# Kernel optimization log

Measured on AMD Instinct MI355X. Metric: run time of the kernel, lower is better.

The kernel has to match this reference:

```python
import jax, jax.numpy as jnp
import numpy as np
import math

# Config (matches init_kwargs): ProphetNet-style ngram self-attention
T, B, E, H, NGRAM, NB, MAXD = 512, 4, 1024, 16, 2, 32, 128
HD = E // H
TGT = (1 + NGRAM) * T
NEG = -1e9


def _buckets(rel):
    # faithful numpy version of _relative_positions_bucket (bidirectional=False)
    n = np.maximum(-rel, 0)
    max_exact = NB // 2
    is_small = n < max_exact
    large = max_exact + np.log(np.maximum(n, 1) / max_exact) / math.log(MAXD / max_exact) * (NB - max_exact)
    large = np.minimum(large, NB - 1).astype(np.int32)
    return np.where(is_small, n.astype(np.int32), large)


def setup_inputs() -> dict:
    key = jax.random.key(0)
    ks = jax.random.split(key, 4)
    s = 0.02
    # position ids 1..T (ProphetNet positions start at 1); precompute bucket tables
    pos = np.arange(1, T + 1, dtype=np.int64)[None, :].repeat(B, axis=0)          # [B,T]
    main_rel = pos[:, None, :] - pos[:, :, None]                                  # [B,T,T]
    pred_keys = np.concatenate([pos - 1, pos], axis=-1)                           # [B,2T]
    pred_rel = pred_keys[:, None, :] - pos[:, :, None]                            # [B,T,2T]
    return {
        "query": jax.random.normal(ks[0], (TGT, B, E), jnp.float32),
        "in_proj_weight": jax.random.normal(ks[1], (3 * E, E), jnp.float32) * s,
        "in_proj_bias": jnp.zeros((3 * E,), jnp.float32),
        "rel_w": jax.random.normal(ks[2], (NB * H, E), jnp.float32) * s,
        "rel_b": jnp.zeros((NB * H,), jnp.float32),
        "out_w": jax.random.normal(ks[3], (E, E), jnp.float32) * s,
        "out_b": jnp.zeros((E,), jnp.float32),
        "main_buckets": jnp.asarray(_buckets(main_rel), jnp.int32),
        "predict_buckets": jnp.asarray(_buckets(pred_rel), jnp.int32),
    }


def reference(query, in_proj_weight, in_proj_bias, rel_w, rel_b, out_w, out_b,
              main_buckets, predict_buckets):
    scaling = HD ** -0.5
    qkv = query @ in_proj_weight.T + in_proj_bias                  # [TGT,B,3E]
    q, k, v = jnp.split(qkv, 3, axis=-1)
    q = q * scaling

    def heads(x):  # [TGT,B,E] -> [B*H, TGT, HD]
        return x.reshape(TGT, B * H, HD).transpose(1, 0, 2)

    q, k, v = heads(q), heads(k), heads(v)
    q_main, k_main, v_main = q[:, :T], k[:, :T], v[:, :T]

    def ngram_split(x):  # [B*H, NGRAM*T, HD] -> [N, B*H, T, HD]
        return x[:, T:].reshape(B * H, NGRAM, T, HD).transpose(1, 0, 2, 3)

    q_pred, k_pred, v_pred = ngram_split(q), ngram_split(k), ngram_split(v)
    h_main = query[:T]                                             # [T,B,E]
    h_pred = query[T:].reshape(NGRAM, T, B, E)

    # ---------- main stream ----------
    aw_main = jnp.einsum('bth,bsh->bts', q_main, k_main)           # [B*H,T,T]
    vals = h_main.transpose(1, 0, 2) @ rel_w.T + rel_b             # [B,T,NB*H]
    vals = vals.reshape(B, T, NB, H).transpose(0, 3, 1, 2)         # [B,H,T,NB]
    idx = jnp.broadcast_to(main_buckets[:, None], (B, H, T, T))
    rel_main = jnp.take_along_axis(vals, idx, axis=-1).reshape(B * H, T, T)
    causal = jnp.triu(jnp.full((T, T), NEG, jnp.float32), 1)       # self_attn_mask
    aw_main = jax.nn.softmax(aw_main + rel_main + causal[None], axis=-1)
    attn_main = jnp.einsum('bts,bsh->bth', aw_main, v_main)        # [B*H,T,HD]
    attn_main = attn_main.transpose(1, 0, 2).reshape(1, T, B, E)
    attn_main = attn_main @ out_w.T + out_b

    # ---------- ngram predict streams ----------
    k_ng = jnp.concatenate([jnp.broadcast_to(k_main[None], (NGRAM, B * H, T, HD)), k_pred], axis=2)
    v_ng = jnp.concatenate([jnp.broadcast_to(v_main[None], (NGRAM, B * H, T, HD)), v_pred], axis=2)
    aw_ng = jnp.einsum('nbtc,nbsc->nbts', q_pred, k_ng)            # [N,B*H,T,2T]
    valsn = h_pred.transpose(0, 2, 1, 3) @ rel_w.T + rel_b         # [N,B,T,NB*H]
    valsn = valsn.reshape(NGRAM, B, T, NB, H).transpose(0, 1, 4, 2, 3)  # [N,B,H,T,NB]
    idxn = jnp.broadcast_to(predict_buckets[None, :, None], (NGRAM, B, H, T, 2 * T))
    rel_ng = jnp.take_along_axis(valsn, idxn, axis=-1).reshape(NGRAM, B * H, T, 2 * T)
    # ngram_mask: main part causal, predict part only the matching position
    ng_mask = jnp.concatenate([causal, NEG * (1.0 - jnp.eye(T, dtype=jnp.float32))], axis=1)  # [T,2T]
    aw_ng = jax.nn.softmax(aw_ng + rel_ng + ng_mask[None, None], axis=-1)
    attn_ng = jnp.einsum('nbts,nbsc->nbtc', aw_ng, v_ng)           # [N,B*H,T,HD]
    attn_ng = attn_ng.transpose(0, 2, 1, 3).reshape(NGRAM, T, B, E)
    attn_ng = attn_ng @ out_w.T + out_b

    return jnp.concatenate([attn_main, attn_ng], axis=0).reshape(TGT, B, E)
```

## Files before the change

kernel.cpp:

```cpp
#include <hip/hip_runtime.h>
#include <hip/hip_bf16.h>
#include <math.h>

constexpr int T_ = 512;
constexpr int B_ = 4;
constexpr int E_ = 1024;
constexpr int H_ = 16;
constexpr int NGRAM_ = 2;
constexpr int TGT_ = (1 + NGRAM_) * T_;
constexpr int ROWS_ = TGT_ * B_;

typedef __bf16 bf16_t;
typedef __bf16 bf16x8 __attribute__((ext_vector_type(8)));
typedef __bf16 bf16x4 __attribute__((ext_vector_type(4)));
typedef float f32x4 __attribute__((ext_vector_type(4)));

#define GLL(gaddr, laddr)                                                     \
  __builtin_amdgcn_global_load_lds(                                           \
      (const __attribute__((address_space(1))) void*)(gaddr),                 \
      (__attribute__((address_space(3))) void*)(laddr), 16, 0, 0)

__global__ __launch_bounds__(256) void prep(
    const float* __restrict__ query, const float* __restrict__ ipw,
    const float* __restrict__ relw, const float* __restrict__ outw,
    bf16_t* __restrict__ qb, bf16_t* __restrict__ ipwb,
    bf16_t* __restrict__ relwb, bf16_t* __restrict__ outwb) {
  const int i = blockIdx.x * 256 + threadIdx.x;
  constexpr int N1 = ROWS_ * E_ / 4;
  constexpr int N2 = 3 * E_ * E_ / 4;
  constexpr int N3 = 512 * E_ / 4;
  constexpr int N4 = E_ * E_ / 4;
  const float4* src;
  bf16_t* dst;
  int j = i;
  if (i < N1) { src = (const float4*)query; dst = qb; }
  else if (i < N1 + N2) { src = (const float4*)ipw; dst = ipwb; j = i - N1; }
  else if (i < N1 + N2 + N3) { src = (const float4*)relw; dst = relwb; j = i - N1 - N2; }
  else if (i < N1 + N2 + N3 + N4) { src = (const float4*)outw; dst = outwb; j = i - N1 - N2 - N3; }
  else return;
  const float4 v = src[j];
  bf16x4 o;
  o[0] = (bf16_t)v.x; o[1] = (bf16_t)v.y;
  o[2] = (bf16_t)v.z; o[3] = (bf16_t)v.w;
  ((bf16x4*)dst)[j] = o;
}

__device__ __forceinline__ int lt_sw(int row, int col) {
  return row * 128 + ((((col >> 3) ^ (row & 15)) << 3) | (col & 7));
}

__global__ __launch_bounds__(256, 4) void bgemm_proj(
    const bf16_t* __restrict__ A, const bf16_t* __restrict__ W,
    const float* __restrict__ ipb, const float* __restrict__ relb,
    bf16_t* __restrict__ qkvb, float* __restrict__ relv2,
    bf16_t* __restrict__ vT) {
  __shared__ bf16_t smem[2 * 128 * 64];
  bf16_t* As = smem;
  bf16_t* Bs = smem + 128 * 64;

  const int tid = threadIdx.x;
  const int wave = tid >> 6, lane = tid & 63;
  const int wr = wave >> 1, wc = wave & 1;
  const int bm = blockIdx.y * 128, bn = blockIdx.x * 128;
  const int q = lane >> 4, ln = lane & 15;
  const int grow = tid >> 3;
  const int gcol = ((tid & 7) ^ (grow & 7)) * 8;

  f32x4 acc[4][4];
#pragma unroll
  for (int mi = 0; mi < 4; ++mi)
#pragma unroll
    for (int ni = 0; ni < 4; ++ni)
#pragma unroll
      for (int r = 0; r < 4; ++r) acc[mi][ni][r] = 0.f;

  const int co[2] = {((q) ^ (ln & 7)) * 8, ((4 + q) ^ (ln & 7)) * 8};

  for (int k0 = 0; k0 < 1024; k0 += 64) {
    __syncthreads();
#pragma unroll
    for (int p = 0; p < 4; ++p) {
      GLL(&A[(size_t)(bm + p * 32 + grow) * 1024 + k0 + gcol], &As[p * 2048 + tid * 8]);
      GLL(&W[(size_t)(bn + p * 32 + grow) * 1024 + k0 + gcol], &Bs[p * 2048 + tid * 8]);
    }
    __syncthreads();
#pragma unroll
    for (int t = 0; t < 2; ++t) {
      bf16x8 af[4], bf[4];
#pragma unroll
      for (int mi = 0; mi < 4; ++mi)
        af[mi] = *(const bf16x8*)&As[(wr * 64 + mi * 16 + ln) * 64 + co[t]];
#pragma unroll
      for (int ni = 0; ni < 4; ++ni)
        bf[ni] = *(const bf16x8*)&Bs[(wc * 64 + ni * 16 + ln) * 64 + co[t]];
#pragma unroll
      for (int mi = 0; mi < 4; ++mi)
#pragma unroll
        for (int ni = 0; ni < 4; ++ni)
          acc[mi][ni] = __builtin_amdgcn_mfma_f32_16x16x32_bf16(
              af[mi], bf[ni], acc[mi][ni], 0, 0, 0);
    }
  }

  if (bn < 2048) {
    const float sc = (bn < 1024) ? 0.125f : 1.0f;
#pragma unroll
    for (int mi = 0; mi < 4; ++mi) {
#pragma unroll
      for (int ni = 0; ni < 4; ++ni) {
        const int col = bn + wc * 64 + ni * 16 + ln;
        const float bv = ipb[col];
#pragma unroll
        for (int r = 0; r < 4; ++r) {
          const int row = bm + wr * 64 + mi * 16 + q * 4 + r;
          qkvb[(size_t)row * 3072 + col] = (bf16_t)((acc[mi][ni][r] + bv) * sc);
        }
      }
    }
  } else if (bn < 3072) {
    __syncthreads();
#pragma unroll
    for (int mi = 0; mi < 4; ++mi) {
#pragma unroll
      for (int ni = 0; ni < 4; ++ni) {
        const int col_l = wc * 64 + ni * 16 + ln;
        const float bv = ipb[bn + col_l];
#pragma unroll
        for (int r = 0; r < 4; ++r) {
          const int row_l = wr * 64 + mi * 16 + q * 4 + r;
          smem[lt_sw(row_l, col_l)] = (bf16_t)(acc[mi][ni][r] + bv);
        }
      }
    }
    __syncthreads();
    const int h0 = (bn - 2048) >> 6;
    const int tb0 = bm >> 2;
#pragma unroll
    for (int e = 0; e < 2; ++e) {
      const int task = tid + e * 256;
      const int b = task & 3;
      const int c = task >> 2;
      const int h = h0 + (c >> 6);
      const int d = c & 63;
      const size_t base = ((size_t)((b * 16 + h) * 64 + d)) * (size_t)TGT_ + tb0;
#pragma unroll
      for (int c4 = 0; c4 < 4; ++c4) {
        bf16x8 v8;
#pragma unroll
        for (int i = 0; i < 8; ++i)
          v8[i] = smem[lt_sw((c4 * 8 + i) * 4 + b, c)];
        *(bf16x8*)&vT[base + c4 * 8] = v8;
      }
    }
  } else {
    const int cb = bn - 3072 + wc * 64;
    float4 rb4;
#pragma unroll
    for (int ni = 0; ni < 4; ++ni)
      ((float*)&rb4)[ni] = relb[cb + ni * 16 + ln];
    const int bkbase = cb >> 4;
#pragma unroll
    for (int mi = 0; mi < 4; ++mi) {
#pragma unroll
      for (int r = 0; r < 4; ++r) {
        const int row = bm + wr * 64 + mi * 16 + q * 4 + r;
        float4 v;
        v.x = acc[mi][0][r] + rb4.x;
        v.y = acc[mi][1][r] + rb4.y;
        v.z = acc[mi][2][r] + rb4.z;
        v.w = acc[mi][3][r] + rb4.w;
        *(float4*)&relv2[(size_t)row * 512 + ln * 32 + bkbase] = v;
      }
    }
  }
}

__global__ __launch_bounds__(256, 4) void bgemm_out(
    const bf16_t* __restrict__ A, const bf16_t* __restrict__ W,
    const float* __restrict__ bias, float* __restrict__ C, int N) {
  __shared__ bf16_t As[128 * 64];
  __shared__ bf16_t Bs[128 * 64];

  const int tid = threadIdx.x;
  const int wave = tid >> 6, lane = tid & 63;
  const int wr = wave >> 1, wc = wave & 1;
  const int bm = blockIdx.y * 128, bn = blockIdx.x * 128;
  const int q = lane >> 4, ln = lane & 15;
  const int grow = tid >> 3;
  const int gcol = ((tid & 7) ^ (grow & 7)) * 8;

  f32x4 acc[4][4];
#pragma unroll
  for (int mi = 0; mi < 4; ++mi)
#pragma unroll
    for (int ni = 0; ni < 4; ++ni)
#pragma unroll
      for (int r = 0; r < 4; ++r) acc[mi][ni][r] = 0.f;

  const int co[2] = {((q) ^ (ln & 7)) * 8, ((4 + q) ^ (ln & 7)) * 8};

  for (int k0 = 0; k0 < 1024; k0 += 64) {
    __syncthreads();
#pragma unroll
    for (int p = 0; p < 4; ++p) {
      GLL(&A[(size_t)(bm + p * 32 + grow) * 1024 + k0 + gcol], &As[p * 2048 + tid * 8]);
      GLL(&W[(size_t)(bn + p * 32 + grow) * 1024 + k0 + gcol], &Bs[p * 2048 + tid * 8]);
    }
    __syncthreads();
#pragma unroll
    for (int t = 0; t < 2; ++t) {
      bf16x8 af[4], bf[4];
#pragma unroll
      for (int mi = 0; mi < 4; ++mi)
        af[mi] = *(const bf16x8*)&As[(wr * 64 + mi * 16 + ln) * 64 + co[t]];
#pragma unroll
      for (int ni = 0; ni < 4; ++ni)
        bf[ni] = *(const bf16x8*)&Bs[(wc * 64 + ni * 16 + ln) * 64 + co[t]];
#pragma unroll
      for (int mi = 0; mi < 4; ++mi)
#pragma unroll
        for (int ni = 0; ni < 4; ++ni)
          acc[mi][ni] = __builtin_amdgcn_mfma_f32_16x16x32_bf16(
              af[mi], bf[ni], acc[mi][ni], 0, 0, 0);
    }
  }

#pragma unroll
  for (int mi = 0; mi < 4; ++mi) {
#pragma unroll
    for (int ni = 0; ni < 4; ++ni) {
      const int col = bn + wc * 64 + ni * 16 + ln;
      const float bv = bias[col];
#pragma unroll
      for (int r = 0; r < 4; ++r) {
        const int row = bm + wr * 64 + mi * 16 + q * 4 + r;
        C[(size_t)row * N + col] = acc[mi][ni][r] + bv;
      }
    }
  }
}

__device__ __forceinline__ int bucket_of(int n) {
  if (n < 16) return n;
  const float lf = __log2f((float)n);
  int b = (int)(16.0f + (lf - 4.0f) * 5.3333333f);
  return b > 31 ? 31 : b;
}

__global__ __launch_bounds__(256, 2) void flash_mfma(
    const bf16_t* __restrict__ qkvb, const bf16_t* __restrict__ vT,
    const float* __restrict__ relv2, bf16_t* __restrict__ attn) {
  __shared__ bf16_t Ks[2][64 * 64];
  __shared__ bf16_t Vts[2][64 * 64];
  __shared__ bf16_t Ps[4][16 * 64];
  __shared__ bf16_t biasS[3][64 * 33];

  const int qt = 7 - blockIdx.x, tq0 = qt * 64;
  const int bh = blockIdx.y, b = bh >> 4, h = bh & 15;
  const int tid = threadIdx.x;
  const int wave = tid >> 6, lane = tid & 63;
  const int q = lane >> 4, ln = lane & 15;
  const int m0 = wave * 16;
  const int grow = tid >> 3;
  const int gcol = ((tid & 7) ^ (grow & 7)) * 8;
  const int co[2] = {((q) ^ (ln & 7)) * 8, ((4 + q) ^ (ln & 7)) * 8};

#pragma unroll
  for (int z = 0; z < 3; ++z) {
#pragma unroll
    for (int u = 0; u < 2; ++u) {
      const int c = u * 256 + tid;
      const int row = c >> 3, j4 = (c & 7) * 4;
      const float4 v = *(const float4*)
          &relv2[((size_t)(z * T_ + tq0 + row) * B_ + b) * 512 + h * 32 + j4];
      biasS[z][row * 33 + j4 + 0] = (bf16_t)v.x;
      biasS[z][row * 33 + j4 + 1] = (bf16_t)v.y;
      biasS[z][row * 33 + j4 + 2] = (bf16_t)v.z;
      biasS[z][row * 33 + j4 + 3] = (bf16_t)v.w;
    }
  }

#pragma unroll
  for (int u = 0; u < 2; ++u) {
    const int sr = u * 32 + grow;
    GLL(&qkvb[((size_t)(0 * T_ + tq0 + sr) * B_ + b) * 3072 + h * 64 + gcol],
        &Ks[0][u * 2048 + tid * 8]);
    GLL(&qkvb[((size_t)(1 * T_ + tq0 + sr) * B_ + b) * 3072 + h * 64 + gcol],
        &Vts[0][u * 2048 + tid * 8]);
    GLL(&qkvb[((size_t)(2 * T_ + tq0 + sr) * B_ + b) * 3072 + h * 64 + gcol],
        &Ks[1][u * 2048 + tid * 8]);
  }
  __syncthreads();

  bf16x8 aq[3][2];
  aq[0][0] = *(const bf16x8*)&Ks[0][(m0 + ln) * 64 + co[0]];
  aq[0][1] = *(const bf16x8*)&Ks[0][(m0 + ln) * 64 + co[1]];
  aq[1][0] = *(const bf16x8*)&Vts[0][(m0 + ln) * 64 + co[0]];
  aq[1][1] = *(const bf16x8*)&Vts[0][(m0 + ln) * 64 + co[1]];
  aq[2][0] = *(const bf16x8*)&Ks[1][(m0 + ln) * 64 + co[0]];
  aq[2][1] = *(const bf16x8*)&Ks[1][(m0 + ln) * 64 + co[1]];

  float bv31[3][4], bv0[3][4];
#pragma unroll
  for (int z = 0; z < 3; ++z)
#pragma unroll
    for (int r = 0; r < 4; ++r) {
      const int rloc = m0 + q * 4 + r;
      bv31[z][r] = (float)biasS[z][rloc * 33 + 31];
      bv0[z][r] = (float)biasS[z][rloc * 33];
    }

  f32x4 Od[3][4];
  float lpart[3][4];
#pragma unroll
  for (int z = 0; z < 3; ++z)
#pragma unroll
    for (int r = 0; r < 4; ++r) {
      lpart[z][r] = 0.f;
#pragma unroll
      for (int tc = 0; tc < 4; ++tc) Od[z][tc][r] = 0.f;
    }

  const int ntiles = qt + 3;

  auto stage_tile = [&](int jj, int buf) {
    const int krb = (jj <= qt) ? jj * 64 : ((jj - qt) * T_ + tq0);
#pragma unroll
    for (int u = 0; u < 2; ++u) {
      const int sr = u * 32 + grow;
      GLL(&qkvb[((size_t)(krb + sr) * B_ + b) * 3072 + 1024 + h * 64 + gcol],
          &Ks[buf][u * 2048 + tid * 8]);
      GLL(&vT[((size_t)bh * 64 + sr) * (size_t)TGT_ + krb + gcol],
          &Vts[buf][u * 2048 + tid * 8]);
    }
  };

  __syncthreads();
  stage_tile(0, 0);
  __syncthreads();

  for (int jj = 0; jj < ntiles; ++jj) {
    const int cur = jj & 1;
    if (jj + 1 < ntiles) stage_tile(jj + 1, cur ^ 1);

    const int krb = (jj <= qt) ? jj * 64 : ((jj - qt) * T_ + tq0);

    bf16x8 kf[4][2], vf[4][2];
#pragma unroll
    for (int tc = 0; tc < 4; ++tc) {
      kf[tc][0] = *(const bf16x8*)&Ks[cur][(tc * 16 + ln) * 64 + co[0]];
      kf[tc][1] = *(const bf16x8*)&Ks[cur][(tc * 16 + ln) * 64 + co[1]];
      vf[tc][0] = *(const bf16x8*)&Vts[cur][(tc * 16 + ln) * 64 + co[0]];
      vf[tc][1] = *(const bf16x8*)&Vts[cur][(tc * 16 + ln) * 64 + co[1]];
    }

    if (jj <= qt) {
      const bool far = (jj <= qt - 3);
#pragma unroll
      for (int z = 0; z < 3; ++z) {
        f32x4 acc[4];
#pragma unroll
        for (int tc = 0; tc < 4; ++tc)
#pragma unroll
          for (int r = 0; r < 4; ++r) acc[tc][r] = 0.f;
#pragma unroll
        for (int tc = 0; tc < 4; ++tc) {
          acc[tc] = __builtin_amdgcn_mfma_f32_16x16x32_bf16(aq[z][0], kf[tc][0], acc[tc], 0, 0, 0);
          acc[tc] = __builtin_amdgcn_mfma_f32_16x16x32_bf16(aq[z][1], kf[tc][1], acc[tc], 0, 0, 0);
        }

        if (far) {
#pragma unroll
          for (int r = 0; r < 4; ++r) {
            const float bv = bv31[z][r];
#pragma unroll
            for (int tc = 0; tc < 4; ++tc) {
              const float p = __expf(acc[tc][r] + bv);
              lpart[z][r] += p;
              const int pc = (tc * 2 + (ln >> 3)) ^ ((q * 4 + r) & 7);
              Ps[wave][(q * 4 + r) * 64 + pc * 8 + (ln & 7)] = (bf16_t)p;
            }
          }
        } else {
#pragma unroll
          for (int r = 0; r < 4; ++r) {
            const int rloc = m0 + q * 4 + r;
            const int dbase = tq0 + rloc - krb;
#pragma unroll
            for (int tc = 0; tc < 4; ++tc) {
              const int sl = tc * 16 + ln;
              const int d = dbase - sl;
              const bool valid = (jj < qt) | (d >= 0);
              int n = d < 0 ? 0 : d;
              if (z > 0) n += 1;
              const float bv = (float)biasS[z][rloc * 33 + bucket_of(n)];
              const float p = valid ? __expf(acc[tc][r] + bv) : 0.f;
              lpart[z][r] += p;
              const int pc = (tc * 2 + (ln >> 3)) ^ ((q * 4 + r) & 7);
              Ps[wave][(q * 4 + r) * 64 + pc * 8 + (ln & 7)] = (bf16_t)p;
            }
          }
        }

        bf16x8 ap[2];
        ap[0] = *(const bf16x8*)&Ps[wave][ln * 64 + co[0]];
        ap[1] = *(const bf16x8*)&Ps[wave][ln * 64 + co[1]];
#pragma unroll
        for (int tc = 0; tc < 4; ++tc) {
          Od[z][tc] = __builtin_amdgcn_mfma_f32_16x16x32_bf16(ap[0], vf[tc][0], Od[z][tc], 0, 0, 0);
          Od[z][tc] = __builtin_amdgcn_mfma_f32_16x16x32_bf16(ap[1], vf[tc][1], Od[z][tc], 0, 0, 0);
        }
      }
    } else {
#pragma unroll
      for (int z = 1; z <= 2; ++z) {
        if (jj - qt == z) {
          f32x4 acc[4];
#pragma unroll
          for (int tc = 0; tc < 4; ++tc)
#pragma unroll
            for (int r = 0; r < 4; ++r) acc[tc][r] = 0.f;
#pragma unroll
          for (int tc = 0; tc < 4; ++tc) {
            acc[tc] = __builtin_amdgcn_mfma_f32_16x16x32_bf16(aq[z][0], kf[tc][0], acc[tc], 0, 0, 0);
            acc[tc] = __builtin_amdgcn_mfma_f32_16x16x32_bf16(aq[z][1], kf[tc][1], acc[tc], 0, 0, 0);
          }
#pragma unroll
          for (int r = 0; r < 4; ++r) {
            const int rloc = m0 + q * 4 + r;
            const float bv = bv0[z][r];
#pragma unroll
            for (int tc = 0; tc < 4; ++tc) {
              const int sl = tc * 16 + ln;
              const float p = (sl == rloc) ? __expf(acc[tc][r] + bv) : 0.f;
              lpart[z][r] += p;
              const int pc = (tc * 2 + (ln >> 3)) ^ ((q * 4 + r) & 7);
              Ps[wave][(q * 4 + r) * 64 + pc * 8 + (ln & 7)] = (bf16_t)p;
            }
          }
          bf16x8 ap[2];
          ap[0] = *(const bf16x8*)&Ps[wave][ln * 64 + co[0]];
          ap[1] = *(const bf16x8*)&Ps[wave][ln * 64 + co[1]];
#pragma unroll
          for (int tc = 0; tc < 4; ++tc) {
            Od[z][tc] = __builtin_amdgcn_mfma_f32_16x16x32_bf16(ap[0], vf[tc][0], Od[z][tc], 0, 0, 0);
            Od[z][tc] = __builtin_amdgcn_mfma_f32_16x16x32_bf16(ap[1], vf[tc][1], Od[z][tc], 0, 0, 0);
          }
        }
      }
    }
    __syncthreads();
  }

#pragma unroll
  for (int z = 0; z < 3; ++z) {
#pragma unroll
    for (int r = 0; r < 4; ++r) {
      float l = lpart[z][r];
      l += __shfl_xor(l, 1, 16);
      l += __shfl_xor(l, 2, 16);
      l += __shfl_xor(l, 4, 16);
      l += __shfl_xor(l, 8, 16);
      const float inv = 1.f / l;
      const size_t rowbase =
          ((size_t)(z * T_ + tq0 + m0 + q * 4 + r) * B_ + b) * (size_t)E_ + h * 64;
#pragma unroll
      for (int tc = 0; tc < 4; ++tc)
        attn[rowbase + tc * 16 + ln] = (bf16_t)(Od[z][tc][r] * inv);
    }
  }
}

extern "C" void kernel_launch(void* const* d_in, const int* in_sizes, int n_in,
                              void* d_out, int out_size, void* d_ws, size_t ws_size,
                              hipStream_t stream) {
  const float* query = (const float*)d_in[0];
  const float* ipw   = (const float*)d_in[1];
  const float* ipb   = (const float*)d_in[2];
  const float* relw  = (const float*)d_in[3];
  const float* relb  = (const float*)d_in[4];
  const float* outw  = (const float*)d_in[5];
  const float* outb  = (const float*)d_in[6];
  float* out = (float*)d_out;

  bf16_t* qkvb  = (bf16_t*)d_ws;
  float*  relv2 = (float*)(qkvb + (size_t)ROWS_ * 3 * E_);
  bf16_t* qb    = (bf16_t*)(relv2 + (size_t)ROWS_ * 512);
  bf16_t* ipwb  = qb + (size_t)ROWS_ * E_;
  bf16_t* relwb = ipwb + (size_t)(3 * E_) * E_;
  bf16_t* outwb = relwb + (size_t)512 * E_;
  bf16_t* attnb = outwb + (size_t)E_ * E_;
  bf16_t* vT    = attnb + (size_t)ROWS_ * E_;

  const dim3 blk(256);

  {
    const int ntot = (ROWS_ * E_ + 3 * E_ * E_ + 512 * E_ + E_ * E_) / 4;
    prep<<<dim3((ntot + 255) / 256), blk, 0, stream>>>(
        query, ipw, relw, outw, qb, ipwb, relwb, outwb);
  }

  bgemm_proj<<<dim3(3584 / 128, ROWS_ / 128), blk, 0, stream>>>(
      qb, ipwb, ipb, relb, qkvb, relv2, vT);

  flash_mfma<<<dim3(8, B_ * H_), blk, 0, stream>>>(
      qkvb, vT, relv2, attnb);

  bgemm_out<<<dim3(E_ / 128, ROWS_ / 128), blk, 0, stream>>>(
      attnb, outwb, outb, out, E_);
}
```

Baseline: 247.6 us.

## Retile projection GEMM to 192x256 with double-buffered LDS and XCD-aware block remap

The QKV/relative projection GEMM moves from 128x128 tiles with 256 threads to 192x256 tiles with 512 threads. It now double-buffers LDS, with async global-to-LDS loads for the next k-tiles overlapping MFMA on the current ones under explicit vmcnt waits. MFMA bursts are interleaved with barriers and setprio. Both GEMMs also get a block-id remap that groups tiles per XCD for better L2 reuse. The cost is larger LDS use (about 112KB) and fewer resident blocks, plus tile-count alignment assumptions (6144/192, 3584/256).

```diff
diff --git a/kernel.cpp b/kernel.cpp
--- a/kernel.cpp
+++ b/kernel.cpp
@@ -19,6 +19,11 @@
   __builtin_amdgcn_global_load_lds(                                           \
       (const __attribute__((address_space(1))) void*)(gaddr),                 \
       (__attribute__((address_space(3))) void*)(laddr), 16, 0, 0)
+
+#define BARX()  asm volatile("s_barrier" ::: "memory")
+#define WVM7()  asm volatile("s_waitcnt vmcnt(7)" ::: "memory")
+#define WVM0()  asm volatile("s_waitcnt vmcnt(0)" ::: "memory")
+#define LGKM0() asm volatile("s_waitcnt lgkmcnt(0)" ::: "memory")
 
 __global__ __launch_bounds__(256) void prep(
     const float* __restrict__ query, const float* __restrict__ ipw,
@@ -45,74 +50,112 @@
   ((bf16x4*)dst)[j] = o;
 }
 
-__device__ __forceinline__ int lt_sw(int row, int col) {
-  return row * 128 + ((((col >> 3) ^ (row & 15)) << 3) | (col & 7));
-}
-
-__global__ __launch_bounds__(256, 4) void bgemm_proj(
+__device__ __forceinline__ int sw256(int row, int col) {
+  return row * 256 + ((((col >> 3) ^ (row & 31)) << 3) | (col & 7));
+}
+
+__global__ __launch_bounds__(512, 2) void bgemm_proj(
     const bf16_t* __restrict__ A, const bf16_t* __restrict__ W,
     const float* __restrict__ ipb, const float* __restrict__ relb,
     bf16_t* __restrict__ qkvb, float* __restrict__ relv2,
     bf16_t* __restrict__ vT) {
-  __shared__ bf16_t smem[2 * 128 * 64];
-  bf16_t* As = smem;
-  bf16_t* Bs = smem + 128 * 64;
+  __shared__ bf16_t smem[57344];
+  bf16_t* As0 = smem;
+  bf16_t* As1 = smem + 12288;
+  bf16_t* Bs0 = smem + 24576;
+  bf16_t* Bs1 = smem + 24576 + 16384;
 
   const int tid = threadIdx.x;
   const int wave = tid >> 6, lane = tid & 63;
-  const int wr = wave >> 1, wc = wave & 1;
-  const int bm = blockIdx.y * 128, bn = blockIdx.x * 128;
+  const int wr = wave >> 2, wc = wave & 3;
+  const int pid = blockIdx.y * 14 + blockIdx.x;
+  const int lid = (pid & 7) * 56 + (pid >> 3);
+  const int by = lid / 14;
+  const int bx = lid - by * 14;
+  const int bm = by * 192, bn = bx * 256;
   const int q = lane >> 4, ln = lane & 15;
   const int grow = tid >> 3;
   const int gcol = ((tid & 7) ^ (grow & 7)) * 8;
-
-  f32x4 acc[4][4];
-#pragma unroll
-  for (int mi = 0; mi < 4; ++mi)
+  const int co[2] = {((q) ^ (ln & 7)) * 8, ((4 + q) ^ (ln & 7)) * 8};
+
+  f32x4 acc[6][4];
+#pragma unroll
+  for (int mi = 0; mi < 6; ++mi)
 #pragma unroll
     for (int ni = 0; ni < 4; ++ni)
 #pragma unroll
       for (int r = 0; r < 4; ++r) acc[mi][ni][r] = 0.f;
 
-  const int co[2] = {((q) ^ (ln & 7)) * 8, ((4 + q) ^ (ln & 7)) * 8};
-
-  for (int k0 = 0; k0 < 1024; k0 += 64) {
-    __syncthreads();
-#pragma unroll
-    for (int p = 0; p < 4; ++p) {
-      GLL(&A[(size_t)(bm + p * 32 + grow) * 1024 + k0 + gcol], &As[p * 2048 + tid * 8]);
-      GLL(&W[(size_t)(bn + p * 32 + grow) * 1024 + k0 + gcol], &Bs[p * 2048 + tid * 8]);
-    }
-    __syncthreads();
+  auto stage = [&](int kt, bf16_t* la, bf16_t* lb) {
+    const int kc = kt * 64 + gcol;
+#pragma unroll
+    for (int p = 0; p < 3; ++p)
+      GLL(&A[(size_t)(bm + p * 64 + grow) * 1024 + kc], &la[p * 4096 + tid * 8]);
+#pragma unroll
+    for (int p = 0; p < 4; ++p)
+      GLL(&W[(size_t)(bn + p * 64 + grow) * 1024 + kc], &lb[p * 4096 + tid * 8]);
+  };
+
+  auto compute = [&](const bf16_t* la, const bf16_t* lb) {
 #pragma unroll
     for (int t = 0; t < 2; ++t) {
-      bf16x8 af[4], bf[4];
-#pragma unroll
-      for (int mi = 0; mi < 4; ++mi)
-        af[mi] = *(const bf16x8*)&As[(wr * 64 + mi * 16 + ln) * 64 + co[t]];
+      bf16x8 bfr[4], afr[3];
 #pragma unroll
       for (int ni = 0; ni < 4; ++ni)
-        bf[ni] = *(const bf16x8*)&Bs[(wc * 64 + ni * 16 + ln) * 64 + co[t]];
-#pragma unroll
-      for (int mi = 0; mi < 4; ++mi)
+        bfr[ni] = *(const bf16x8*)&lb[(wc * 64 + ni * 16 + ln) * 64 + co[t]];
+#pragma unroll
+      for (int mi = 0; mi < 3; ++mi)
+        afr[mi] = *(const bf16x8*)&la[(wr * 96 + mi * 16 + ln) * 64 + co[t]];
+      BARX(); LGKM0();
+      __builtin_amdgcn_s_setprio(1);
+#pragma unroll
+      for (int mi = 0; mi < 3; ++mi)
 #pragma unroll
         for (int ni = 0; ni < 4; ++ni)
           acc[mi][ni] = __builtin_amdgcn_mfma_f32_16x16x32_bf16(
-              af[mi], bf[ni], acc[mi][ni], 0, 0, 0);
-    }
+              afr[mi], bfr[ni], acc[mi][ni], 0, 0, 0);
+      __builtin_amdgcn_s_setprio(0);
+      BARX();
+#pragma unroll
+      for (int mi = 0; mi < 3; ++mi)
+        afr[mi] = *(const bf16x8*)&la[(wr * 96 + (3 + mi) * 16 + ln) * 64 + co[t]];
+      BARX(); LGKM0();
+      __builtin_amdgcn_s_setprio(1);
+#pragma unroll
+      for (int mi = 0; mi < 3; ++mi)
+#pragma unroll
+        for (int ni = 0; ni < 4; ++ni)
+          acc[3 + mi][ni] = __builtin_amdgcn_mfma_f32_16x16x32_bf16(
+              afr[mi], bfr[ni], acc[3 + mi][ni], 0, 0, 0);
+      __builtin_amdgcn_s_setprio(0);
+      BARX();
+    }
+  };
+
+  stage(0, As0, Bs0);
+  stage(1, As1, Bs1);
+
+  for (int jj = 0; jj < 8; ++jj) {
+    WVM7(); BARX();
+    compute(As0, Bs0);
+    if (jj < 7) stage(2 * jj + 2, As0, Bs0);
+    if (jj < 7) { WVM7(); } else { WVM0(); }
+    BARX();
+    compute(As1, Bs1);
+    if (jj < 7) stage(2 * jj + 3, As1, Bs1);
   }
 
   if (bn < 2048) {
     const float sc = (bn < 1024) ? 0.125f : 1.0f;
 #pragma unroll
-    for (int mi = 0; mi < 4; ++mi) {
+    for (int mi = 0; mi < 6; ++mi) {
 #pragma unroll
       for (int ni = 0; ni < 4; ++ni) {
         const int col = bn + wc * 64 + ni * 16 + ln;
         const float bv = ipb[col];
 #pragma unroll
         for (int r = 0; r < 4; ++r) {
-          const int row = bm + wr * 64 + mi * 16 + q * 4 + r;
+          const int row = bm + wr * 96 + mi * 16 + q * 4 + r;
           qkvb[(size_t)row * 3072 + col] = (bf16_t)((acc[mi][ni][r] + bv) * sc);
         }
       }
@@ -120,15 +163,15 @@
   } else if (bn < 3072) {
     __syncthreads();
 #pragma unroll
-    for (int mi = 0; mi < 4; ++mi) {
+    for (int mi = 0; mi < 6; ++mi) {
 #pragma unroll
       for (int ni = 0; ni < 4; ++ni) {
         const int col_l = wc * 64 + ni * 16 + ln;
         const float bv = ipb[bn + col_l];
 #pragma unroll
         for (int r = 0; r < 4; ++r) {
-          const int row_l = wr * 64 + mi * 16 + q * 4 + r;
-          smem[lt_sw(row_l, col_l)] = (bf16_t)(acc[mi][ni][r] + bv);
+          const int row_l = wr * 96 + mi * 16 + q * 4 + r;
+          smem[sw256(row_l, col_l)] = (bf16_t)(acc[mi][ni][r] + bv);
         }
       }
     }
@@ -137,19 +180,19 @@
     const int tb0 = bm >> 2;
 #pragma unroll
     for (int e = 0; e < 2; ++e) {
-      const int task = tid + e * 256;
+      const int task = e * 512 + tid;
       const int b = task & 3;
       const int c = task >> 2;
       const int h = h0 + (c >> 6);
       const int d = c & 63;
       const size_t base = ((size_t)((b * 16 + h) * 64 + d)) * (size_t)TGT_ + tb0;
 #pragma unroll
-      for (int c4 = 0; c4 < 4; ++c4) {
+      for (int k = 0; k < 6; ++k) {
         bf16x8 v8;
 #pragma unroll
         for (int i = 0; i < 8; ++i)
-          v8[i] = smem[lt_sw((c4 * 8 + i) * 4 + b, c)];
-        *(bf16x8*)&vT[base + c4 * 8] = v8;
+          v8[i] = smem[sw256((k * 8 + i) * 4 + b, c)];
+        *(bf16x8*)&vT[base + k * 8] = v8;
       }
     }
   } else {
@@ -160,10 +203,10 @@
       ((float*)&rb4)[ni] = relb[cb + ni * 16 + ln];
     const int bkbase = cb >> 4;
 #pragma unroll
-    for (int mi = 0; mi < 4; ++mi) {
+    for (int mi = 0; mi < 6; ++mi) {
 #pragma unroll
       for (int r = 0; r < 4; ++r) {
-        const int row = bm + wr * 64 + mi * 16 + q * 4 + r;
+        const int row = bm + wr * 96 + mi * 16 + q * 4 + r;
         float4 v;
         v.x = acc[mi][0][r] + rb4.x;
         v.y = acc[mi][1][r] + rb4.y;
@@ -184,7 +227,9 @@
   const int tid = threadIdx.x;
   const int wave = tid >> 6, lane = tid & 63;
   const int wr = wave >> 1, wc = wave & 1;
-  const int bm = blockIdx.y * 128, bn = blockIdx.x * 128;
+  const int pid = blockIdx.y * 8 + blockIdx.x;
+  const int lid = (pid & 7) * 48 + (pid >> 3);
+  const int bm = (lid >> 3) * 128, bn = (lid & 7) * 128;
   const int q = lane >> 4, ln = lane & 15;
   const int grow = tid >> 3;
   const int gcol = ((tid & 7) ^ (grow & 7)) * 8;
@@ -500,7 +545,7 @@
         query, ipw, relw, outw, qb, ipwb, relwb, outwb);
   }
 
-  bgemm_proj<<<dim3(3584 / 128, ROWS_ / 128), blk, 0, stream>>>(
+  bgemm_proj<<<dim3(3584 / 256, ROWS_ / 192), dim3(512), 0, stream>>>(
       qb, ipwb, ipb, relb, qkvb, relv2, vT);
 
   flash_mfma<<<dim3(8, B_ * H_), blk, 0, stream>>>(
```

Result: faster. 240.6 us (-2.8%).
